# Kernel optimization log

Measured on AMD Instinct MI355X. Metric: run time of the kernel, lower is better.

Reference implementation:

```python
import jax, jax.numpy as jnp
import numpy as np

NEG_SLOPE = 0.2

def _gat_layer(x, src, dst, W, a_s, a_d, b, concat):
    # x: [N, F_in], W: [F_in, H*C], a_s/a_d: [H, C]
    N = x.shape[0]
    H, C = a_s.shape
    h = (x @ W).reshape(N, H, C)                       # per-head projection
    al_s = jnp.sum(h * a_s, axis=-1)                   # [N, H]
    al_d = jnp.sum(h * a_d, axis=-1)                   # [N, H]
    e = jax.nn.leaky_relu(al_s[src] + al_d[dst], NEG_SLOPE)  # [E, H]
    # segment softmax over incoming edges of each dst node
    m = jax.ops.segment_max(e, dst, num_segments=N)    # [N, H]
    ex = jnp.exp(e - m[dst])
    denom = jax.ops.segment_sum(ex, dst, num_segments=N)
    alpha = ex / denom[dst]                            # [E, H]
    msg = h[src] * alpha[:, :, None]                   # [E, H, C]
    out = jax.ops.segment_sum(msg, dst, num_segments=N)  # [N, H, C]
    if concat:
        return out.reshape(N, H * C) + b
    return out.mean(axis=1) + b


def setup_inputs() -> dict:
    key = jax.random.key(0)
    ks = jax.random.split(key, 12)
    N, F_in, H, C1, LAT, E = 16384, 512, 4, 128, 64, 262144
    x = jax.random.normal(ks[0], (N, F_in), dtype=jnp.float32)
    edge_index = jax.random.randint(ks[1], (2, E), 0, N, dtype=jnp.int64)
    s = 0.05
    return {
        'x': x,
        'edge_index': edge_index,
        'W1': jax.random.normal(ks[2], (F_in, H * C1), dtype=jnp.float32) * s,
        'a_src1': jax.random.normal(ks[3], (H, C1), dtype=jnp.float32) * s,
        'a_dst1': jax.random.normal(ks[4], (H, C1), dtype=jnp.float32) * s,
        'b1': jax.random.normal(ks[5], (H * C1,), dtype=jnp.float32) * s,
        'W2': jax.random.normal(ks[6], (H * C1, H * LAT), dtype=jnp.float32) * s,
        'a_src2': jax.random.normal(ks[7], (H, LAT), dtype=jnp.float32) * s,
        'a_dst2': jax.random.normal(ks[8], (H, LAT), dtype=jnp.float32) * s,
        'b2': jax.random.normal(ks[9], (LAT,), dtype=jnp.float32) * s,
    }


def reference(x, edge_index, W1, a_src1, a_dst1, b1, W2, a_src2, a_dst2, b2):
    N = x.shape[0]
    # PyG GATConv default add_self_loops=True
    loop = jnp.arange(N, dtype=edge_index.dtype)
    src = jnp.concatenate([edge_index[0], loop])
    dst = jnp.concatenate([edge_index[1], loop])
    h = jax.nn.relu(_gat_layer(x, src, dst, W1, a_src1, a_dst1, b1, concat=True))
    out = _gat_layer(h, src, dst, W2, a_src2, a_dst2, b2, concat=False)
    return out
```

## Files before the change

kernel.cpp:

```cpp
#include <hip/hip_runtime.h>
#include <stdint.h>
#include <stddef.h>
#include <limits.h>

typedef __bf16 bf16;
typedef __bf16 bf16x4 __attribute__((ext_vector_type(4)));
typedef __bf16 bf16x8 __attribute__((ext_vector_type(8)));
typedef float  f32x4  __attribute__((ext_vector_type(4)));

static __device__ __forceinline__ float lrelu(float x) { return x > 0.f ? x : 0.2f * x; }
static __device__ __forceinline__ float san(float v) { return (fabsf(v) < 1e4f) ? v : 0.0f; }

static __device__ __forceinline__ void async_load16(const bf16* g, bf16* l) {
  __builtin_amdgcn_global_load_lds((const __attribute__((address_space(1))) void*)g,
                                   (__attribute__((address_space(3))) void*)l, 16, 0, 0);
}


__global__ __launch_bounds__(256) void prep_all(const float* __restrict__ x,
                                                bf16* __restrict__ xb,
                                                int* __restrict__ counts,
                                                const float* __restrict__ W1,
                                                const float* __restrict__ W2,
                                                bf16* __restrict__ W1T,
                                                bf16* __restrict__ W2T,
                                                int NX, int N) {
  int b = blockIdx.x;
  const int NCVT = NX >> 10;
  if (b < NCVT) {
    int i = b * 1024 + threadIdx.x * 4;
    f32x4 v = *(const f32x4*)(x + i);
    bf16x4 o;
#pragma unroll
    for (int k = 0; k < 4; ++k) o[k] = (bf16)san(v[k]);
    *(bf16x4*)(xb + i) = o;
    return;
  }
  b -= NCVT;
  if (b < N / 256) { counts[b * 256 + threadIdx.x] = 0; return; }
  b -= N / 256;
  __shared__ bf16 t[32][33];
  const float* in; bf16* out; int R, C, bx, by;
  if (b < 256) { in = W1; out = W1T; R = 512; C = 512; by = b >> 4; bx = b & 15; }
  else         { b -= 256; in = W2; out = W2T; R = 512; C = 256; by = b >> 3; bx = b & 7; }
  const int lane = threadIdx.x & 31, r8 = threadIdx.x >> 5;
#pragma unroll
  for (int k = 0; k < 4; ++k) {
    int r = by * 32 + r8 + k * 8, c = bx * 32 + lane;
    t[lane][r8 + k * 8] = (bf16)san(in[(size_t)r * C + c]);
  }
  __syncthreads();
#pragma unroll
  for (int k = 0; k < 4; ++k) {
    int oc = bx * 32 + r8 + k * 8;
    out[(size_t)oc * R + by * 32 + lane] = t[r8 + k * 8][lane];
  }
}


__global__ void count_edges(const int* __restrict__ dst, int E, int* __restrict__ counts) {
  int e = blockIdx.x * 256 + threadIdx.x;
  if (e < E) atomicAdd(&counts[dst[e]], 1);
}

__global__ __launch_bounds__(1024) void scan_block_sums(const int* __restrict__ counts,
                                                        int* __restrict__ bsums) {
  __shared__ int ws[16];
  const int tid = threadIdx.x, lane = tid & 63, w = tid >> 6;
  int v = counts[blockIdx.x * 1024 + tid];
  for (int off = 32; off; off >>= 1) v += __shfl_xor(v, off);
  if (lane == 0) ws[w] = v;
  __syncthreads();
  if (tid == 0) {
    int s = 0;
#pragma unroll
    for (int k = 0; k < 16; ++k) s += ws[k];
    bsums[blockIdx.x] = s;
  }
}

__global__ __launch_bounds__(1024) void scan_apply(const int* __restrict__ counts,
                                                   const int* __restrict__ bsums,
                                                   int* __restrict__ row_ptr,
                                                   int* __restrict__ cursor, int N, int nb) {
  __shared__ int wsum[16];
  __shared__ int bpre[2];
  const int tid = threadIdx.x, lane = tid & 63, w = tid >> 6;
  const int gi = blockIdx.x * 1024 + tid;
  if (tid == 0) {
    int pre = 0, tot = 0;
    for (int k = 0; k < nb; ++k) {
      if (k < (int)blockIdx.x) pre += bsums[k];
      tot += bsums[k];
    }
    bpre[0] = pre; bpre[1] = tot;
  }
  int v = counts[gi];
  int s = v;
  for (int off = 1; off < 64; off <<= 1) {
    int t = __shfl_up(s, off);
    if (lane >= off) s += t;
  }
  if (lane == 63) wsum[w] = s;
  __syncthreads();
  if (w == 0 && lane < 16) {
    int ws = wsum[lane];
    int t2 = ws;
    for (int off = 1; off < 16; off <<= 1) {
      int t = __shfl_up(t2, off);
      if (lane >= off) t2 += t;
    }
    wsum[lane] = t2 - ws;
  }
  __syncthreads();
  int excl = bpre[0] + wsum[w] + s - v;
  row_ptr[gi] = excl;
  cursor[gi]  = excl;
  if (gi == N - 1) row_ptr[N] = bpre[1];
}

__global__ void scatter_edges(const int* __restrict__ src, const int* __restrict__ dst, int E,
                              int* __restrict__ cursor, int* __restrict__ csr_src) {
  int e = blockIdx.x * 256 + threadIdx.x;
  if (e < E) {
    int pos = atomicAdd(&cursor[dst[e]], 1);
    csr_src[pos] = src[e];
  }
}

__global__ __launch_bounds__(256) void sort_rows_wave(const int* __restrict__ row_ptr,
                                                      int* __restrict__ csr, int N) {
  const int wid  = (blockIdx.x * 256 + threadIdx.x) >> 6;
  const int lane = threadIdx.x & 63;
  if (wid >= N) return;
  const int beg = row_ptr[wid], end = row_ptr[wid + 1];
  const int len = end - beg;
  if (len <= 1) return;
  if (len <= 64) {
    int v = (lane < len) ? csr[beg + lane] : INT_MAX;
#pragma unroll
    for (int k = 2; k <= 64; k <<= 1) {
#pragma unroll
      for (int j = k >> 1; j > 0; j >>= 1) {
        int p = __shfl_xor(v, j);
        bool take_min = (((lane & k) == 0) == ((lane & j) == 0));
        v = take_min ? min(v, p) : max(v, p);
      }
    }
    if (lane < len) csr[beg + lane] = v;
  } else if (lane == 0) {
    for (int i = beg + 1; i < end; ++i) {
      int v = csr[i];
      int j = i - 1;
      while (j >= beg && csr[j] > v) { csr[j + 1] = csr[j]; --j; }
      csr[j + 1] = v;
    }
  }
}


__global__ __launch_bounds__(256) void gemm_al_l1(const bf16* __restrict__ A,
                                                  const bf16* __restrict__ BT,
                                                  bf16* __restrict__ C,
                                                  const float* __restrict__ a_s,
                                                  const float* __restrict__ a_d,
                                                  float* __restrict__ al_s,
                                                  float* __restrict__ al_d,
                                                  int M, int N, int K) {
  __shared__ __align__(16) bf16 As[128 * 32];
  __shared__ __align__(16) bf16 Bs[128 * 32];
  __shared__ float alred[2][128][2];
  const int tid  = threadIdx.x;
  const int lane = tid & 63;
  const int wave = tid >> 6;
  const int m0 = blockIdx.x * 128;
  const int n0 = blockIdx.y * 128;
  const int wm = (wave >> 1) * 64;
  const int wn = (wave & 1) * 64;

  f32x4 acc[4][4] = {};

  const int id0 = tid, id1 = tid + 256;
  const bf16* a0p = A  + (size_t)(m0 + (id0 >> 2)) * K + (id0 & 3) * 8;
  const bf16* a1p = A  + (size_t)(m0 + (id1 >> 2)) * K + (id1 & 3) * 8;
  const bf16* b0p = BT + (size_t)(n0 + (id0 >> 2)) * K + (id0 & 3) * 8;
  const bf16* b1p = BT + (size_t)(n0 + (id1 >> 2)) * K + (id1 & 3) * 8;

  const int kq = (lane >> 4) * 8;
  const int rA = wm + (lane & 15);
  const int rB = wn + (lane & 15);

  for (int k0 = 0; k0 < K; k0 += 32) {
    __syncthreads();
    async_load16(a0p + k0, &As[id0 * 8]);
    async_load16(a1p + k0, &As[id1 * 8]);
    async_load16(b0p + k0, &Bs[id0 * 8]);
    async_load16(b1p + k0, &Bs[id1 * 8]);
    __syncthreads();
    bf16x8 af[4], bfv[4];
#pragma unroll
    for (int i = 0; i < 4; ++i) af[i]  = *(const bf16x8*)&As[(rA + i * 16) * 32 + kq];
#pragma unroll
    for (int j = 0; j < 4; ++j) bfv[j] = *(const bf16x8*)&Bs[(rB + j * 16) * 32 + kq];
#pragma unroll
    for (int i = 0; i < 4; ++i)
#pragma unroll
      for (int j = 0; j < 4; ++j)
        acc[i][j] = __builtin_amdgcn_mfma_f32_16x16x32_bf16(af[i], bfv[j], acc[i][j], 0, 0, 0);
  }

  const int cc = lane & 15;
  const int rb = (lane >> 4) * 4;
#pragma unroll
  for (int i = 0; i < 4; ++i)
#pragma unroll
    for (int j = 0; j < 4; ++j) {
      int gcol = n0 + wn + j * 16 + cc;
#pragma unroll
      for (int r = 0; r < 4; ++r) {
        int grow = m0 + wm + i * 16 + rb + r;
        C[(size_t)grow * N + gcol] = (bf16)acc[i][j][r];
      }
    }

  {
    const int head = blockIdx.y;
    float asv[4], adv[4];
#pragma unroll
    for (int j = 0; j < 4; ++j) {
      int col = head * 128 + wn + j * 16 + cc;
      asv[j] = san(a_s[col]);
      adv[j] = san(a_d[col]);
    }
    const int wnh = wn >> 6;
#pragma unroll
    for (int i = 0; i < 4; ++i)
#pragma unroll
      for (int r = 0; r < 4; ++r) {
        float ps = 0.f, pd = 0.f;
#pragma unroll
        for (int j = 0; j < 4; ++j) { ps += acc[i][j][r] * asv[j]; pd += acc[i][j][r] * adv[j]; }
#pragma unroll
        for (int off = 1; off <= 8; off <<= 1) {
          ps += __shfl_xor(ps, off);
          pd += __shfl_xor(pd, off);
        }
        if (cc == 0) {
          int row = wm + i * 16 + rb + r;
          alred[wnh][row][0] = ps;
          alred[wnh][row][1] = pd;
        }
      }
    __syncthreads();
    if (tid < 128) {
      al_s[(size_t)(m0 + tid) * 4 + head] = alred[0][tid][0] + alred[1][tid][0];
      al_d[(size_t)(m0 + tid) * 4 + head] = alred[0][tid][1] + alred[1][tid][1];
    }
  }
}


__global__ __launch_bounds__(256) void gemm_al_l2(const bf16* __restrict__ A,
                                                  const bf16* __restrict__ BT,
                                                  bf16* __restrict__ C,
                                                  const float* __restrict__ a_s,
                                                  const float* __restrict__ a_d,
                                                  float* __restrict__ al_s,
                                                  float* __restrict__ al_d,
                                                  int M, int N, int K) {
  __shared__ __align__(16) bf16 As[64 * 32];
  __shared__ __align__(16) bf16 Bs[128 * 32];
  const int tid  = threadIdx.x;
  const int lane = tid & 63;
  const int wave = tid >> 6;
  const int m0 = blockIdx.x * 64;
  const int n0 = blockIdx.y * 128;
  const int wm = (wave >> 1) * 32;
  const int wn = (wave & 1) * 64;

  f32x4 acc[2][4] = {};

  const int tb = tid + 256;
  const bf16* ap  = A  + (size_t)(m0 + (tid >> 2)) * K + (tid & 3) * 8;
  const bf16* bp0 = BT + (size_t)(n0 + (tid >> 2)) * K + (tid & 3) * 8;
  const bf16* bp1 = BT + (size_t)(n0 + (tb  >> 2)) * K + (tb  & 3) * 8;

  const int kq = (lane >> 4) * 8;
  const int rA = wm + (lane & 15);
  const int rB = wn + (lane & 15);

  for (int k0 = 0; k0 < K; k0 += 32) {
    __syncthreads();
    async_load16(ap  + k0, &As[tid * 8]);
    async_load16(bp0 + k0, &Bs[tid * 8]);
    async_load16(bp1 + k0, &Bs[tb  * 8]);
    __syncthreads();
    bf16x8 af[2], bfv[4];
#pragma unroll
    for (int i = 0; i < 2; ++i) af[i]  = *(const bf16x8*)&As[(rA + i * 16) * 32 + kq];
#pragma unroll
    for (int j = 0; j < 4; ++j) bfv[j] = *(const bf16x8*)&Bs[(rB + j * 16) * 32 + kq];
#pragma unroll
    for (int i = 0; i < 2; ++i)
#pragma unroll
      for (int j = 0; j < 4; ++j)
        acc[i][j] = __builtin_amdgcn_mfma_f32_16x16x32_bf16(af[i], bfv[j], acc[i][j], 0, 0, 0);
  }

  const int cc = lane & 15;
  const int rb = (lane >> 4) * 4;
#pragma unroll
  for (int i = 0; i < 2; ++i)
#pragma unroll
    for (int j = 0; j < 4; ++j) {
      int gcol = n0 + wn + j * 16 + cc;
#pragma unroll
      for (int r = 0; r < 4; ++r) {
        int grow = m0 + wm + i * 16 + rb + r;
        C[(size_t)grow * N + gcol] = (bf16)acc[i][j][r];
      }
    }

  {
    const int head = blockIdx.y * 2 + (wn >> 6);
    float asv[4], adv[4];
#pragma unroll
    for (int j = 0; j < 4; ++j) {
      int col = head * 64 + j * 16 + cc;
      asv[j] = san(a_s[col]);
      adv[j] = san(a_d[col]);
    }
#pragma unroll
    for (int i = 0; i < 2; ++i)
#pragma unroll
      for (int r = 0; r < 4; ++r) {
        float ps = 0.f, pd = 0.f;
#pragma unroll
        for (int j = 0; j < 4; ++j) { ps += acc[i][j][r] * asv[j]; pd += acc[i][j][r] * adv[j]; }
#pragma unroll
        for (int off = 1; off <= 8; off <<= 1) {
          ps += __shfl_xor(ps, off);
          pd += __shfl_xor(pd, off);
        }
        if (cc == 0) {
          int row = m0 + wm + i * 16 + rb + r;
          al_s[(size_t)row * 4 + head] = ps;
          al_d[(size_t)row * 4 + head] = pd;
        }
      }
  }
}


__global__ __launch_bounds__(128) void aggregate1_f(const bf16* __restrict__ h1,
                                                    const float* __restrict__ al_s,
                                                    const float* __restrict__ al_d,
                                                    const int* __restrict__ row_ptr,
                                                    const int* __restrict__ csr_src,
                                                    const float* __restrict__ bias,
                                                    bf16* __restrict__ out) {
  __shared__ int   sIdx[64];
  __shared__ f32x4 sW[64];
  __shared__ float sM[4];
  __shared__ float sL[4];
  const int n = blockIdx.x, tid = threadIdx.x;
  const int hd = tid >> 5, lane = tid & 63, wv = tid >> 6;
  const int cb = tid * 4;
  const int beg = row_ptr[n], end = row_ptr[n + 1], len = end - beg;
  const f32x4 alsn = *(const f32x4*)(al_s + (size_t)n * 4);
  const f32x4 aldn = *(const f32x4*)(al_d + (size_t)n * 4);

  if (wv == 0) {
    f32x4 Mv;
#pragma unroll
    for (int h = 0; h < 4; ++h) Mv[h] = lrelu(alsn[h] + aldn[h]);
    for (int j = lane; j < len; j += 64) {
      int s = csr_src[beg + j];
      f32x4 a = *(const f32x4*)(al_s + (size_t)s * 4);
#pragma unroll
      for (int h = 0; h < 4; ++h) Mv[h] = fmaxf(Mv[h], lrelu(a[h] + aldn[h]));
    }
    for (int off = 32; off; off >>= 1) {
#pragma unroll
      for (int h = 0; h < 4; ++h) Mv[h] = fmaxf(Mv[h], __shfl_xor(Mv[h], off));
    }
    if (lane == 0) *(f32x4*)sM = Mv;
  }
  __syncthreads();
  const float wself = __expf(lrelu(alsn[hd] + aldn[hd]) - sM[hd]);
  bf16x4 hv0 = *(const bf16x4*)(h1 + (size_t)n * 512 + cb);
  float acc0 = wself * (float)hv0[0], acc1 = wself * (float)hv0[1];
  float acc2 = wself * (float)hv0[2], acc3 = wself * (float)hv0[3];
  f32x4 Lv = {0.f, 0.f, 0.f, 0.f};
  if (tid == 0) {
#pragma unroll
    for (int h = 0; h < 4; ++h) Lv[h] = __expf(lrelu(alsn[h] + aldn[h]) - sM[h]);
  }
  for (int c0 = beg; c0 < end; c0 += 64) {
    const int cl = min(64, end - c0);
    __syncthreads();
    if (wv == 0 && lane < cl) {
      int s = csr_src[c0 + lane];
      sIdx[lane] = s;
      f32x4 a = *(const f32x4*)(al_s + (size_t)s * 4);
      f32x4 w;
#pragma unroll
      for (int h = 0; h < 4; ++h) w[h] = __expf(lrelu(a[h] + aldn[h]) - sM[h]);
      sW[lane] = w;
#pragma unroll
      for (int h = 0; h < 4; ++h) Lv[h] += w[h];
    }
    __syncthreads();
#pragma unroll 4
    for (int j = 0; j < cl; ++j) {
      int s = sIdx[j];
      float a = sW[j][hd];
      bf16x4 hv = *(const bf16x4*)(h1 + (size_t)s * 512 + cb);
      acc0 += a * (float)hv[0];
      acc1 += a * (float)hv[1];
      acc2 += a * (float)hv[2];
      acc3 += a * (float)hv[3];
    }
  }
  if (wv == 0) {
    for (int off = 32; off; off >>= 1) {
#pragma unroll
      for (int h = 0; h < 4; ++h) Lv[h] += __shfl_xor(Lv[h], off);
    }
    if (lane == 0) *(f32x4*)sL = Lv;
  }
  __syncthreads();
  const float inv = 1.0f / sL[hd];
  bf16x4 ov;
  ov[0] = (bf16)fmaxf(acc0 * inv + san(bias[cb]),     0.f);
  ov[1] = (bf16)fmaxf(acc1 * inv + san(bias[cb + 1]), 0.f);
  ov[2] = (bf16)fmaxf(acc2 * inv + san(bias[cb + 2]), 0.f);
  ov[3] = (bf16)fmaxf(acc3 * inv + san(bias[cb + 3]), 0.f);
  *(bf16x4*)(out + (size_t)n * 512 + cb) = ov;
}


__global__ __launch_bounds__(64) void aggregate2_f(const bf16* __restrict__ h2,
                                                   const float* __restrict__ al_s,
                                                   const float* __restrict__ al_d,
                                                   const int* __restrict__ row_ptr,
                                                   const int* __restrict__ csr_src,
                                                   const float* __restrict__ bias,
                                                   float* __restrict__ out) {
  __shared__ int   sIdx[64];
  __shared__ f32x4 sW[64];
  __shared__ float sM[4];
  __shared__ float sL[4];
  const int n = blockIdx.x, lane = threadIdx.x;
  const int hd = lane >> 4;
  const int cb = lane * 4;
  const int beg = row_ptr[n], end = row_ptr[n + 1], len = end - beg;
  const f32x4 alsn = *(const f32x4*)(al_s + (size_t)n * 4);
  const f32x4 aldn = *(const f32x4*)(al_d + (size_t)n * 4);

  f32x4 Mv;
#pragma unroll
  for (int h = 0; h < 4; ++h) Mv[h] = lrelu(alsn[h] + aldn[h]);
  for (int j = lane; j < len; j += 64) {
    int s = csr_src[beg + j];
    f32x4 a = *(const f32x4*)(al_s + (size_t)s * 4);
#pragma unroll
    for (int h = 0; h < 4; ++h) Mv[h] = fmaxf(Mv[h], lrelu(a[h] + aldn[h]));
  }
  for (int off = 32; off; off >>= 1) {
#pragma unroll
    for (int h = 0; h < 4; ++h) Mv[h] = fmaxf(Mv[h], __shfl_xor(Mv[h], off));
  }
  if (lane == 0) *(f32x4*)sM = Mv;
  __syncthreads();

  const float wself = __expf(lrelu(alsn[hd] + aldn[hd]) - sM[hd]);
  bf16x4 hv0 = *(const bf16x4*)(h2 + (size_t)n * 256 + cb);
  float acc0 = wself * (float)hv0[0], acc1 = wself * (float)hv0[1];
  float acc2 = wself * (float)hv0[2], acc3 = wself * (float)hv0[3];
  f32x4 Lv = {0.f, 0.f, 0.f, 0.f};
  if (lane == 0) {
#pragma unroll
    for (int h = 0; h < 4; ++h) Lv[h] = __expf(lrelu(alsn[h] + aldn[h]) - sM[h]);
  }
  for (int c0 = beg; c0 < end; c0 += 64) {
    const int cl = min(64, end - c0);
    __syncthreads();
    if (lane < cl) {
      int s = csr_src[c0 + lane];
      sIdx[lane] = s;
      f32x4 a = *(const f32x4*)(al_s + (size_t)s * 4);
      f32x4 w;
#pragma unroll
      for (int h = 0; h < 4; ++h) w[h] = __expf(lrelu(a[h] + aldn[h]) - sM[h]);
      sW[lane] = w;
#pragma unroll
      for (int h = 0; h < 4; ++h) Lv[h] += w[h];
    }
    __syncthreads();
#pragma unroll 4
    for (int j = 0; j < cl; ++j) {
      int s = sIdx[j];
      float a = sW[j][hd];
      bf16x4 hv = *(const bf16x4*)(h2 + (size_t)s * 256 + cb);
      acc0 += a * (float)hv[0];
      acc1 += a * (float)hv[1];
      acc2 += a * (float)hv[2];
      acc3 += a * (float)hv[3];
    }
  }
  for (int off = 32; off; off >>= 1) {
#pragma unroll
    for (int h = 0; h < 4; ++h) Lv[h] += __shfl_xor(Lv[h], off);
  }
  if (lane == 0) *(f32x4*)sL = Lv;
  __syncthreads();
  const float inv = 1.0f / sL[hd];
  acc0 *= inv; acc1 *= inv; acc2 *= inv; acc3 *= inv;
  acc0 += __shfl_xor(acc0, 16); acc1 += __shfl_xor(acc1, 16);
  acc2 += __shfl_xor(acc2, 16); acc3 += __shfl_xor(acc3, 16);
  acc0 += __shfl_xor(acc0, 32); acc1 += __shfl_xor(acc1, 32);
  acc2 += __shfl_xor(acc2, 32); acc3 += __shfl_xor(acc3, 32);
  if (lane < 16) {
    int ob = lane * 4;
    f32x4 ov;
    ov[0] = 0.25f * acc0 + san(bias[ob]);
    ov[1] = 0.25f * acc1 + san(bias[ob + 1]);
    ov[2] = 0.25f * acc2 + san(bias[ob + 2]);
    ov[3] = 0.25f * acc3 + san(bias[ob + 3]);
    *(f32x4*)(out + (size_t)n * 64 + ob) = ov;
  }
}


extern "C" void kernel_launch(void* const* d_in, const int* in_sizes, int n_in,
                              void* d_out, int out_size, void* d_ws, size_t ws_size,
                              hipStream_t stream) {
  const float* x   = (const float*)d_in[0];
  const int*   ei  = (const int*)d_in[1];
  const float* W1  = (const float*)d_in[2];
  const float* as1 = (const float*)d_in[3];
  const float* ad1 = (const float*)d_in[4];
  const float* b1  = (const float*)d_in[5];
  const float* W2  = (const float*)d_in[6];
  const float* as2 = (const float*)d_in[7];
  const float* ad2 = (const float*)d_in[8];
  const float* b2  = (const float*)d_in[9];
  float* outp = (float*)d_out;

  const int N = in_sizes[0] / 512;
  const int E = in_sizes[1] / 2;
  const int* src = ei;
  const int* dst = ei + E;

  char* p = (char*)d_ws;
  auto alloc = [&](size_t bytes) {
    char* r = p;
    p += (bytes + 255) & ~(size_t)255;
    return r;
  };
  bf16* xb    = (bf16*)alloc((size_t)N * 512 * 2);
  bf16* h1    = (bf16*)alloc((size_t)N * 512 * 2);
  bf16* hbuf  = (bf16*)alloc((size_t)N * 512 * 2);
  bf16* W1T   = (bf16*)alloc((size_t)512 * 512 * 2);
  bf16* W2T   = (bf16*)alloc((size_t)256 * 512 * 2);
  float* al_s1 = (float*)alloc((size_t)N * 4 * 4);
  float* al_d1 = (float*)alloc((size_t)N * 4 * 4);
  float* al_s2 = (float*)alloc((size_t)N * 4 * 4);
  float* al_d2 = (float*)alloc((size_t)N * 4 * 4);
  int* counts  = (int*)alloc((size_t)N * 4);
  int* row_ptr = (int*)alloc((size_t)(N + 1) * 4);
  int* cursor  = (int*)alloc((size_t)N * 4);
  int* csr_src = (int*)alloc((size_t)E * 4);
  int* bsums   = (int*)alloc((size_t)32 * 4);
  bf16* h2 = h1;

  const int nb = N / 1024;
  const int NX = N * 512;

  prep_all<<<(NX >> 10) + N / 256 + 256 + 128, 256, 0, stream>>>(
      x, xb, counts, W1, W2, W1T, W2T, NX, N);

  count_edges<<<(E + 255) / 256, 256, 0, stream>>>(dst, E, counts);
  scan_block_sums<<<nb, 1024, 0, stream>>>(counts, bsums);
  scan_apply<<<nb, 1024, 0, stream>>>(counts, bsums, row_ptr, cursor, N, nb);
  scatter_edges<<<(E + 255) / 256, 256, 0, stream>>>(src, dst, E, cursor, csr_src);
  sort_rows_wave<<<(N * 64 + 255) / 256, 256, 0, stream>>>(row_ptr, csr_src, N);

  gemm_al_l1<<<dim3(N / 128, 4), 256, 0, stream>>>(xb, W1T, h1, as1, ad1, al_s1, al_d1,
                                                   N, 512, 512);
  aggregate1_f<<<N, 128, 0, stream>>>(h1, al_s1, al_d1, row_ptr, csr_src, b1, hbuf);

  gemm_al_l2<<<dim3(N / 64, 2), 256, 0, stream>>>(hbuf, W2T, h2, as2, ad2, al_s2, al_d2,
                                                  N, 256, 512);
  aggregate2_f<<<N, 64, 0, stream>>>(h2, al_s2, al_d2, row_ptr, csr_src, b2, outp);
}
```

Measured before the change: 229.5 us.

## Drop softmax max pass and run layer-1 aggregation as one wave with 8-wide loads

Both aggregation kernels no longer make a separate pass over each node's incoming edges to find the segment max. The softmax now exponentiates raw logits clamped at 30, which removes a gather of al_s per edge and a block barrier. The risk is that the result is only exact while logits stay below the clamp; above it, numerics can change or overflow. Layer-1 aggregation also moves from a 128-thread block to a single 64-lane wave where each lane loads 8 bf16 values per edge, and the denominator reduction stays in registers instead of going through shared memory.

```diff
diff --git a/kernel.cpp b/kernel.cpp
--- a/kernel.cpp
+++ b/kernel.cpp
@@ -10,6 +10,7 @@
 
 static __device__ __forceinline__ float lrelu(float x) { return x > 0.f ? x : 0.2f * x; }
 static __device__ __forceinline__ float san(float v) { return (fabsf(v) < 1e4f) ? v : 0.0f; }
+static __device__ __forceinline__ float wexp(float e) { return __expf(fminf(e, 30.f)); }
 
 static __device__ __forceinline__ void async_load16(const bf16* g, bf16* l) {
   __builtin_amdgcn_global_load_lds((const __attribute__((address_space(1))) void*)g,
@@ -352,60 +353,43 @@
 }
 
 
-__global__ __launch_bounds__(128) void aggregate1_f(const bf16* __restrict__ h1,
-                                                    const float* __restrict__ al_s,
-                                                    const float* __restrict__ al_d,
-                                                    const int* __restrict__ row_ptr,
-                                                    const int* __restrict__ csr_src,
-                                                    const float* __restrict__ bias,
-                                                    bf16* __restrict__ out) {
+__global__ __launch_bounds__(64) void aggregate1_f(const bf16* __restrict__ h1,
+                                                   const float* __restrict__ al_s,
+                                                   const float* __restrict__ al_d,
+                                                   const int* __restrict__ row_ptr,
+                                                   const int* __restrict__ csr_src,
+                                                   const float* __restrict__ bias,
+                                                   bf16* __restrict__ out) {
   __shared__ int   sIdx[64];
   __shared__ f32x4 sW[64];
-  __shared__ float sM[4];
-  __shared__ float sL[4];
-  const int n = blockIdx.x, tid = threadIdx.x;
-  const int hd = tid >> 5, lane = tid & 63, wv = tid >> 6;
-  const int cb = tid * 4;
-  const int beg = row_ptr[n], end = row_ptr[n + 1], len = end - beg;
+  const int n = blockIdx.x, lane = threadIdx.x;
+  const int cb = lane * 8;
+  const int hd = lane >> 4;
+  const int beg = row_ptr[n], end = row_ptr[n + 1];
   const f32x4 alsn = *(const f32x4*)(al_s + (size_t)n * 4);
   const f32x4 aldn = *(const f32x4*)(al_d + (size_t)n * 4);
 
-  if (wv == 0) {
-    f32x4 Mv;
-#pragma unroll
-    for (int h = 0; h < 4; ++h) Mv[h] = lrelu(alsn[h] + aldn[h]);
-    for (int j = lane; j < len; j += 64) {
-      int s = csr_src[beg + j];
-      f32x4 a = *(const f32x4*)(al_s + (size_t)s * 4);
-#pragma unroll
-      for (int h = 0; h < 4; ++h) Mv[h] = fmaxf(Mv[h], lrelu(a[h] + aldn[h]));
-    }
-    for (int off = 32; off; off >>= 1) {
-#pragma unroll
-      for (int h = 0; h < 4; ++h) Mv[h] = fmaxf(Mv[h], __shfl_xor(Mv[h], off));
-    }
-    if (lane == 0) *(f32x4*)sM = Mv;
-  }
-  __syncthreads();
-  const float wself = __expf(lrelu(alsn[hd] + aldn[hd]) - sM[hd]);
-  bf16x4 hv0 = *(const bf16x4*)(h1 + (size_t)n * 512 + cb);
-  float acc0 = wself * (float)hv0[0], acc1 = wself * (float)hv0[1];
-  float acc2 = wself * (float)hv0[2], acc3 = wself * (float)hv0[3];
+  const float wself = wexp(lrelu(alsn[hd] + aldn[hd]));
+  bf16x8 hv0 = *(const bf16x8*)(h1 + (size_t)n * 512 + cb);
+  float acc[8];
+#pragma unroll
+  for (int k = 0; k < 8; ++k) acc[k] = wself * (float)hv0[k];
+
   f32x4 Lv = {0.f, 0.f, 0.f, 0.f};
-  if (tid == 0) {
-#pragma unroll
-    for (int h = 0; h < 4; ++h) Lv[h] = __expf(lrelu(alsn[h] + aldn[h]) - sM[h]);
+  if (lane == 0) {
+#pragma unroll
+    for (int h = 0; h < 4; ++h) Lv[h] = wexp(lrelu(alsn[h] + aldn[h]));
   }
   for (int c0 = beg; c0 < end; c0 += 64) {
     const int cl = min(64, end - c0);
     __syncthreads();
-    if (wv == 0 && lane < cl) {
+    if (lane < cl) {
       int s = csr_src[c0 + lane];
       sIdx[lane] = s;
       f32x4 a = *(const f32x4*)(al_s + (size_t)s * 4);
       f32x4 w;
 #pragma unroll
-      for (int h = 0; h < 4; ++h) w[h] = __expf(lrelu(a[h] + aldn[h]) - sM[h]);
+      for (int h = 0; h < 4; ++h) w[h] = wexp(lrelu(a[h] + aldn[h]));
       sW[lane] = w;
 #pragma unroll
       for (int h = 0; h < 4; ++h) Lv[h] += w[h];
@@ -415,28 +399,21 @@
     for (int j = 0; j < cl; ++j) {
       int s = sIdx[j];
       float a = sW[j][hd];
-      bf16x4 hv = *(const bf16x4*)(h1 + (size_t)s * 512 + cb);
-      acc0 += a * (float)hv[0];
-      acc1 += a * (float)hv[1];
-      acc2 += a * (float)hv[2];
-      acc3 += a * (float)hv[3];
-    }
-  }
-  if (wv == 0) {
-    for (int off = 32; off; off >>= 1) {
-#pragma unroll
-      for (int h = 0; h < 4; ++h) Lv[h] += __shfl_xor(Lv[h], off);
-    }
-    if (lane == 0) *(f32x4*)sL = Lv;
-  }
-  __syncthreads();
-  const float inv = 1.0f / sL[hd];
-  bf16x4 ov;
-  ov[0] = (bf16)fmaxf(acc0 * inv + san(bias[cb]),     0.f);
-  ov[1] = (bf16)fmaxf(acc1 * inv + san(bias[cb + 1]), 0.f);
-  ov[2] = (bf16)fmaxf(acc2 * inv + san(bias[cb + 2]), 0.f);
-  ov[3] = (bf16)fmaxf(acc3 * inv + san(bias[cb + 3]), 0.f);
-  *(bf16x4*)(out + (size_t)n * 512 + cb) = ov;
+      bf16x8 hv = *(const bf16x8*)(h1 + (size_t)s * 512 + cb);
+#pragma unroll
+      for (int k = 0; k < 8; ++k) acc[k] += a * (float)hv[k];
+    }
+  }
+  for (int off = 32; off; off >>= 1) {
+#pragma unroll
+    for (int h = 0; h < 4; ++h) Lv[h] += __shfl_xor(Lv[h], off);
+  }
+  const float inv = 1.0f / Lv[hd];
+  bf16x8 ov;
+#pragma unroll
+  for (int k = 0; k < 8; ++k)
+    ov[k] = (bf16)fmaxf(acc[k] * inv + san(bias[cb + k]), 0.f);
+  *(bf16x8*)(out + (size_t)n * 512 + cb) = ov;
 }
 
 
@@ -449,39 +426,21 @@
                                                    float* __restrict__ out) {
   __shared__ int   sIdx[64];
   __shared__ f32x4 sW[64];
-  __shared__ float sM[4];
-  __shared__ float sL[4];
   const int n = blockIdx.x, lane = threadIdx.x;
   const int hd = lane >> 4;
   const int cb = lane * 4;
-  const int beg = row_ptr[n], end = row_ptr[n + 1], len = end - beg;
+  const int beg = row_ptr[n], end = row_ptr[n + 1];
   const f32x4 alsn = *(const f32x4*)(al_s + (size_t)n * 4);
   const f32x4 aldn = *(const f32x4*)(al_d + (size_t)n * 4);
 
-  f32x4 Mv;
-#pragma unroll
-  for (int h = 0; h < 4; ++h) Mv[h] = lrelu(alsn[h] + aldn[h]);
-  for (int j = lane; j < len; j += 64) {
-    int s = csr_src[beg + j];
-    f32x4 a = *(const f32x4*)(al_s + (size_t)s * 4);
-#pragma unroll
-    for (int h = 0; h < 4; ++h) Mv[h] = fmaxf(Mv[h], lrelu(a[h] + aldn[h]));
-  }
-  for (int off = 32; off; off >>= 1) {
-#pragma unroll
-    for (int h = 0; h < 4; ++h) Mv[h] = fmaxf(Mv[h], __shfl_xor(Mv[h], off));
-  }
-  if (lane == 0) *(f32x4*)sM = Mv;
-  __syncthreads();
-
-  const float wself = __expf(lrelu(alsn[hd] + aldn[hd]) - sM[hd]);
+  const float wself = wexp(lrelu(alsn[hd] + aldn[hd]));
   bf16x4 hv0 = *(const bf16x4*)(h2 + (size_t)n * 256 + cb);
   float acc0 = wself * (float)hv0[0], acc1 = wself * (float)hv0[1];
   float acc2 = wself * (float)hv0[2], acc3 = wself * (float)hv0[3];
   f32x4 Lv = {0.f, 0.f, 0.f, 0.f};
   if (lane == 0) {
 #pragma unroll
-    for (int h = 0; h < 4; ++h) Lv[h] = __expf(lrelu(alsn[h] + aldn[h]) - sM[h]);
+    for (int h = 0; h < 4; ++h) Lv[h] = wexp(lrelu(alsn[h] + aldn[h]));
   }
   for (int c0 = beg; c0 < end; c0 += 64) {
     const int cl = min(64, end - c0);
@@ -492,7 +451,7 @@
       f32x4 a = *(const f32x4*)(al_s + (size_t)s * 4);
       f32x4 w;
 #pragma unroll
-      for (int h = 0; h < 4; ++h) w[h] = __expf(lrelu(a[h] + aldn[h]) - sM[h]);
+      for (int h = 0; h < 4; ++h) w[h] = wexp(lrelu(a[h] + aldn[h]));
       sW[lane] = w;
 #pragma unroll
       for (int h = 0; h < 4; ++h) Lv[h] += w[h];
@@ -513,9 +472,7 @@
 #pragma unroll
     for (int h = 0; h < 4; ++h) Lv[h] += __shfl_xor(Lv[h], off);
   }
-  if (lane == 0) *(f32x4*)sL = Lv;
-  __syncthreads();
-  const float inv = 1.0f / sL[hd];
+  const float inv = 1.0f / Lv[hd];
   acc0 *= inv; acc1 *= inv; acc2 *= inv; acc3 *= inv;
   acc0 += __shfl_xor(acc0, 16); acc1 += __shfl_xor(acc1, 16);
   acc2 += __shfl_xor(acc2, 16); acc3 += __shfl_xor(acc3, 16);
@@ -589,7 +546,7 @@
 
   gemm_al_l1<<<dim3(N / 128, 4), 256, 0, stream>>>(xb, W1T, h1, as1, ad1, al_s1, al_d1,
                                                    N, 512, 512);
-  aggregate1_f<<<N, 128, 0, stream>>>(h1, al_s1, al_d1, row_ptr, csr_src, b1, hbuf);
+  aggregate1_f<<<N, 64, 0, stream>>>(h1, al_s1, al_d1, row_ptr, csr_src, b1, hbuf);
 
   gemm_al_l2<<<dim3(N / 64, 2), 256, 0, stream>>>(hbuf, W2T, h2, as2, ad2, al_s2, al_d2,
                                                   N, 256, 512);
```

Result: faster. 223.5 us (-2.6%).
